# Performance work log

Hardware: AMD Instinct MI355X
Metric: run time of the kernel (lower is better)

Reference implementation:

```python
import jax, jax.numpy as jnp
import numpy as np

NODES_PER_GRAPH = 116
HEADS = 2
D_HEAD = 116  # out_channels per head
HID = 256
B = 512
N = B * NODES_PER_GRAPH
DEG = 8
E = N * DEG
D_OUT = HEADS * D_HEAD  # 232


def setup_inputs() -> dict:
    key = jax.random.key(0)
    ks = jax.random.split(key, 6)
    h_flat = jax.random.normal(ks[0], (N, HID), dtype=jnp.float32)
    # every node receives DEG edges from random nodes within its own 116-node graph
    dst = jnp.repeat(jnp.arange(N, dtype=jnp.int64), DEG)
    offs = jax.random.randint(ks[1], (E,), 0, NODES_PER_GRAPH, dtype=jnp.int64)
    src = (dst // NODES_PER_GRAPH) * NODES_PER_GRAPH + offs
    edge_index = jnp.stack([src, dst], axis=0)
    batch_index = jnp.repeat(jnp.arange(B, dtype=jnp.int64), NODES_PER_GRAPH)
    s = 1.0 / np.sqrt(HID)
    Wq = jax.random.normal(ks[2], (HID, D_OUT), dtype=jnp.float32) * s
    Wk = jax.random.normal(ks[3], (HID, D_OUT), dtype=jnp.float32) * s
    Wv = jax.random.normal(ks[4], (HID, D_OUT), dtype=jnp.float32) * s
    Ws = jax.random.normal(ks[5], (HID, D_OUT), dtype=jnp.float32) * s
    return {"h_flat": h_flat, "edge_index": edge_index, "batch_index": batch_index,
            "Wq": Wq, "Wk": Wk, "Wv": Wv, "Ws": Ws}


def _graph_transformer_layer(h, edge_index, Wq, Wk, Wv, Ws):
    # PyG TransformerConv-style multi-head edge attention, concat heads + root skip.
    n = h.shape[0]
    q = (h @ Wq).reshape(n, HEADS, D_HEAD)
    k = (h @ Wk).reshape(n, HEADS, D_HEAD)
    v = (h @ Wv).reshape(n, HEADS, D_HEAD)
    src, dst = edge_index[0], edge_index[1]
    # per-edge scores [E, H]
    scores = jnp.einsum('ehd,ehd->eh', q[dst], k[src]) / np.sqrt(D_HEAD)
    # segment softmax over incoming edges of each dst node
    m = jax.ops.segment_max(scores, dst, num_segments=n)
    m = jnp.where(jnp.isfinite(m), m, 0.0)
    ex = jnp.exp(scores - m[dst])
    denom = jax.ops.segment_sum(ex, dst, num_segments=n)
    alpha_e = ex / (denom[dst] + 1e-16)
    msg = alpha_e[:, :, None] * v[src]                      # [E, H, Dh]
    attn = jax.ops.segment_sum(msg, dst, num_segments=n)    # [N, H, Dh]
    return attn.reshape(n, D_OUT) + h @ Ws


def reference(h_flat, edge_index, batch_index, Wq, Wk, Wv, Ws):
    n = h_flat.shape[0]
    b = n // NODES_PER_GRAPH
    h_proj = _graph_transformer_layer(h_flat, edge_index, Wq, Wk, Wv, Ws)  # [N, 232]
    e = h_proj.mean(axis=-1)                                 # [N]
    # scatter_softmax over per-graph node segments
    em = jax.ops.segment_max(e, batch_index, num_segments=b)
    ee = jnp.exp(e - em[batch_index])
    es = jax.ops.segment_sum(ee, batch_index, num_segments=b)
    alpha = ee / es[batch_index]                             # [N]
    h_weighted = alpha[:, None] * h_proj                     # [N, 232]
    alpha_map = alpha.reshape(b, NODES_PER_GRAPH)            # [B, 116]
    return alpha_map, h_weighted
```

## Files before the change

### kernel.cpp

```cpp
#include <hip/hip_runtime.h>

#define NODES  116
#define HEADS  2
#define DH     116
#define HID    256
#define NGRAPH 512
#define NN     (NGRAPH*NODES)
#define DEG    8
#define DOUT   (HEADS*DH)
#define RSTR   136

typedef short  s8v  __attribute__((ext_vector_type(8)));
typedef float  f4v  __attribute__((ext_vector_type(4)));

static __device__ __forceinline__ float bf2f(unsigned short u) {
    union { unsigned int i; float f; } c; c.i = ((unsigned int)u) << 16; return c.f;
}
static __device__ __forceinline__ unsigned short f2bf(float f) {
    union { float f; unsigned int u; } c; c.f = f;
    unsigned int u = c.u;
    unsigned int r = (u + 0x7FFFu + ((u >> 16) & 1u)) >> 16;
    return (unsigned short)r;
}

#define GLD_LDS16(gptr, lptr) \
    __builtin_amdgcn_global_load_lds((const __attribute__((address_space(1))) void*)(gptr), \
                                     (__attribute__((address_space(3))) void*)(lptr), 16, 0, 0)

__global__ __launch_bounds__(256) void prep_w(const float* __restrict__ Wq,
                                              const float* __restrict__ Wk,
                                              const float* __restrict__ Wv,
                                              const float* __restrict__ Ws,
                                              unsigned short* __restrict__ wt)
{
    unsigned int f = blockIdx.x * 256 + threadIdx.x;
    unsigned int n    = f & 127;
    unsigned int quad = (f >> 7) & 3;
    unsigned int kb   = (f >> 9) & 7;
    unsigned int ch   = (f >> 12) & 3;
    unsigned int hd   = f >> 14;
    unsigned short o[8] = {0,0,0,0,0,0,0,0};
    if (n < NODES) {
        unsigned int col = hd * DH + n;
        unsigned int k   = kb * 32 + quad * 8;
        const float* W = (ch == 0) ? Wq : (ch == 1) ? Wk : (ch == 2) ? Wv : Ws;
        #pragma unroll
        for (int i = 0; i < 8; i++)
            o[i] = f2bf(W[(size_t)(k + i) * DOUT + col]);
    }
    *(uint4*)(wt + (size_t)f * 8) = *(const uint4*)o;
}

__global__ __launch_bounds__(1024) void fused_all(
    const float* __restrict__ h,
    const unsigned short* __restrict__ wt,
    const int* __restrict__ eidx,
    unsigned short* __restrict__ hp,
    float* __restrict__ out_alpha,
    float* __restrict__ out_hw)
{
    __shared__ __align__(16) unsigned short stA[2*4096];
    __shared__ __align__(16) unsigned short stB[2*16384];
    __shared__ __align__(16) unsigned short ql[128*RSTR];
    __shared__ __align__(16) unsigned short kl[128*RSTR];
    __shared__ int   srcl[NODES*DEG];
    __shared__ float scf[NODES*DEG];
    __shared__ float ps[2][NODES];
    __shared__ float red[2];

    const int g   = blockIdx.x;
    const int tid = threadIdx.x;
    const int w    = tid >> 6;
    const int lane = tid & 63;
    const int l15  = lane & 15;
    const int quad = lane >> 4;
    const int wm   = w >> 2;
    const int wn   = w & 3;

    if (tid < NODES * DEG)
        srcl[tid] = eidx[(size_t)g * NODES * DEG + tid] - g * NODES;

    const int am = tid >> 3;
    const int q8 = tid & 7;
    long grow = (long)g * NODES + am;
    if (grow >= NN) grow = NN - 1;
    const float* hrow = h + (size_t)grow * HID + q8 * 4;
    const int aoff = ((q8 >> 1) * 128 + am) * 8 + (q8 & 1) * 4;

    for (int hd = 0; hd < 2; hd++) {
        const size_t wbase = (size_t)hd * 4 * 8 * 4096;

        f4v accq[2][2], acck[2][2], accv[2][2], accs[2][2];
        #pragma unroll
        for (int i = 0; i < 2; i++)
            #pragma unroll
            for (int j = 0; j < 2; j++)
                #pragma unroll
                for (int r = 0; r < 4; r++) {
                    accq[i][j][r] = 0.f; acck[i][j][r] = 0.f;
                    accv[i][j][r] = 0.f; accs[i][j][r] = 0.f;
                }

        {
            float4 av = *(const float4*)(hrow);
            #pragma unroll
            for (int j = 0; j < 2; j++) {
                int c = w * 2 + j;
                int ch = c >> 3, sub = c & 7;
                const unsigned short* src = wt + wbase + ((size_t)(ch * 8 + 0)) * 4096 + sub * 512;
                GLD_LDS16((const char*)src + lane * 16, (char*)stB + c * 1024);
            }
            unsigned short o[4] = { f2bf(av.x), f2bf(av.y), f2bf(av.z), f2bf(av.w) };
            *(uint2*)(stA + aoff) = *(const uint2*)o;
        }
        __syncthreads();

        int cur = 0;
        for (int kb = 0; kb < 8; kb++) {
            float4 av;
            if (kb < 7) {
                av = *(const float4*)(hrow + (kb + 1) * 32);
                #pragma unroll
                for (int j = 0; j < 2; j++) {
                    int c = w * 2 + j;
                    int ch = c >> 3, sub = c & 7;
                    const unsigned short* src = wt + wbase + ((size_t)(ch * 8 + kb + 1)) * 4096 + sub * 512;
                    GLD_LDS16((const char*)src + lane * 16,
                              (char*)stB + (cur ^ 1) * 32768 + c * 1024);
                }
            }
            const unsigned short* sa = stA + cur * 4096;
            const unsigned short* sb = stB + cur * 16384;
            s8v a0 = *(const s8v*)(sa + (quad * 128 + wm * 32 + l15) * 8);
            s8v a1 = *(const s8v*)(sa + (quad * 128 + wm * 32 + 16 + l15) * 8);
            #pragma unroll
            for (int ch = 0; ch < 4; ch++) {
                s8v b0 = *(const s8v*)(sb + ch * 4096 + (quad * 128 + wn * 32 + l15) * 8);
                s8v b1 = *(const s8v*)(sb + ch * 4096 + (quad * 128 + wn * 32 + 16 + l15) * 8);
                f4v (*acc)[2] = (ch == 0) ? accq : (ch == 1) ? acck : (ch == 2) ? accv : accs;
                acc[0][0] = __builtin_amdgcn_mfma_f32_16x16x32_bf16(a0, b0, acc[0][0], 0, 0, 0);
                acc[0][1] = __builtin_amdgcn_mfma_f32_16x16x32_bf16(a0, b1, acc[0][1], 0, 0, 0);
                acc[1][0] = __builtin_amdgcn_mfma_f32_16x16x32_bf16(a1, b0, acc[1][0], 0, 0, 0);
                acc[1][1] = __builtin_amdgcn_mfma_f32_16x16x32_bf16(a1, b1, acc[1][1], 0, 0, 0);
            }
            if (kb < 7) {
                unsigned short o[4] = { f2bf(av.x), f2bf(av.y), f2bf(av.z), f2bf(av.w) };
                *(uint2*)(stA + (cur ^ 1) * 4096 + aoff) = *(const uint2*)o;
            }
            __syncthreads();
            cur ^= 1;
        }

        #pragma unroll
        for (int i = 0; i < 2; i++) {
            #pragma unroll
            for (int j = 0; j < 2; j++) {
                int col = wn * 32 + j * 16 + l15;
                #pragma unroll
                for (int r = 0; r < 4; r++) {
                    int row = wm * 32 + i * 16 + quad * 4 + r;
                    ql[row * RSTR + col] = (col < NODES) ? f2bf(accq[i][j][r]) : 0;
                    kl[row * RSTR + col] = (col < NODES) ? f2bf(acck[i][j][r]) : 0;
                }
            }
        }
        __syncthreads();

        f4v sacc[2][2];
        #pragma unroll
        for (int i = 0; i < 2; i++)
            #pragma unroll
            for (int j = 0; j < 2; j++)
                #pragma unroll
                for (int r = 0; r < 4; r++) sacc[i][j][r] = 0.f;
        #pragma unroll
        for (int ks = 0; ks < 4; ks++) {
            s8v a0 = *(const s8v*)(ql + (wm * 32 + l15) * RSTR + ks * 32 + quad * 8);
            s8v a1 = *(const s8v*)(ql + (wm * 32 + 16 + l15) * RSTR + ks * 32 + quad * 8);
            s8v b0 = *(const s8v*)(kl + (wn * 32 + l15) * RSTR + ks * 32 + quad * 8);
            s8v b1 = *(const s8v*)(kl + (wn * 32 + 16 + l15) * RSTR + ks * 32 + quad * 8);
            sacc[0][0] = __builtin_amdgcn_mfma_f32_16x16x32_bf16(a0, b0, sacc[0][0], 0, 0, 0);
            sacc[0][1] = __builtin_amdgcn_mfma_f32_16x16x32_bf16(a0, b1, sacc[0][1], 0, 0, 0);
            sacc[1][0] = __builtin_amdgcn_mfma_f32_16x16x32_bf16(a1, b0, sacc[1][0], 0, 0, 0);
            sacc[1][1] = __builtin_amdgcn_mfma_f32_16x16x32_bf16(a1, b1, sacc[1][1], 0, 0, 0);
        }
        #pragma unroll
        for (int i = 0; i < 2; i++) {
            #pragma unroll
            for (int r = 0; r < 4; r++) {
                int row = wm * 32 + i * 16 + quad * 4 + r;
                if (row < NODES) {
                    #pragma unroll
                    for (int j = 0; j < 2; j++) {
                        int col = wn * 32 + j * 16 + l15;
                        #pragma unroll
                        for (int e = 0; e < DEG; e++)
                            if (srcl[row * DEG + e] == col)
                                scf[row * DEG + e] = sacc[i][j][r];
                    }
                }
            }
        }
        __syncthreads();

        for (int f = tid; f < 128 * RSTR / 8; f += 1024)
            *(uint4*)(kl + (size_t)f * 8) = make_uint4(0u, 0u, 0u, 0u);
        #pragma unroll
        for (int i = 0; i < 2; i++) {
            #pragma unroll
            for (int j = 0; j < 2; j++) {
                int col = wn * 32 + j * 16 + l15;
                #pragma unroll
                for (int r = 0; r < 4; r++) {
                    int row = wm * 32 + i * 16 + quad * 4 + r;
                    ql[col * RSTR + row] = (row < NODES) ? f2bf(accv[i][j][r]) : 0;
                }
            }
        }
        __syncthreads();

        if (tid < NODES * DEG) {
            float s = scf[tid] * 0.09284766908852594f;
            float m = s;
            m = fmaxf(m, __shfl_xor(m, 1));
            m = fmaxf(m, __shfl_xor(m, 2));
            m = fmaxf(m, __shfl_xor(m, 4));
            float e = __expf(s - m);
            float sum = e;
            sum += __shfl_xor(sum, 1);
            sum += __shfl_xor(sum, 2);
            sum += __shfl_xor(sum, 4);
            scf[tid] = e / sum;
        }
        __syncthreads();

        if (tid < NODES) {
            #pragma unroll
            for (int j = 0; j < DEG; j++) {
                int sj = srcl[tid * DEG + j];
                bool first = true;
                for (int jj = 0; jj < j; jj++) first = first && (srcl[tid * DEG + jj] != sj);
                if (first) {
                    float a = scf[tid * DEG + j];
                    for (int jj = j + 1; jj < DEG; jj++)
                        if (srcl[tid * DEG + jj] == sj) a += scf[tid * DEG + jj];
                    kl[tid * RSTR + sj] = f2bf(a);
                }
            }
        }
        __syncthreads();

        #pragma unroll
        for (int ks = 0; ks < 4; ks++) {
            s8v a0 = *(const s8v*)(kl + (wm * 32 + l15) * RSTR + ks * 32 + quad * 8);
            s8v a1 = *(const s8v*)(kl + (wm * 32 + 16 + l15) * RSTR + ks * 32 + quad * 8);
            s8v b0 = *(const s8v*)(ql + (wn * 32 + l15) * RSTR + ks * 32 + quad * 8);
            s8v b1 = *(const s8v*)(ql + (wn * 32 + 16 + l15) * RSTR + ks * 32 + quad * 8);
            accs[0][0] = __builtin_amdgcn_mfma_f32_16x16x32_bf16(a0, b0, accs[0][0], 0, 0, 0);
            accs[0][1] = __builtin_amdgcn_mfma_f32_16x16x32_bf16(a0, b1, accs[0][1], 0, 0, 0);
            accs[1][0] = __builtin_amdgcn_mfma_f32_16x16x32_bf16(a1, b0, accs[1][0], 0, 0, 0);
            accs[1][1] = __builtin_amdgcn_mfma_f32_16x16x32_bf16(a1, b1, accs[1][1], 0, 0, 0);
        }
        __syncthreads();

        #pragma unroll
        for (int i = 0; i < 2; i++) {
            #pragma unroll
            for (int j = 0; j < 2; j++) {
                int col = wn * 32 + j * 16 + l15;
                #pragma unroll
                for (int r = 0; r < 4; r++) {
                    int row = wm * 32 + i * 16 + quad * 4 + r;
                    ql[row * RSTR + col] = f2bf(accs[i][j][r]);
                }
            }
        }
        __syncthreads();

        if (tid < NODES * DEG) {
            const int i   = tid >> 3;
            const int seg = tid & 7;
            float rs = 0.0f;
            #pragma unroll
            for (int t = 0; t < 2; t++) {
                int gi = seg + t * 8;
                if (gi < 15) {
                    const s8v v8 = *(const s8v*)(ql + i * RSTR + gi * 8);
                    #pragma unroll
                    for (int e = 0; e < 8; e++) rs += bf2f((unsigned short)v8[e]);
                }
            }
            rs += __shfl_xor(rs, 1);
            rs += __shfl_xor(rs, 2);
            rs += __shfl_xor(rs, 4);
            if (seg == 0) ps[hd][i] = rs;
        }
        if (hd == 0) {
            for (int f = tid; f < NODES * 29; f += 1024) {
                int r  = f / 29;
                int gi = f - r * 29;
                *(uint2*)(hp + ((size_t)g * NODES + r) * 116 + gi * 4) =
                    *(const uint2*)(ql + r * RSTR + gi * 4);
            }
        }
        __syncthreads();
    }

    if (tid < NODES) scf[tid] = (ps[0][tid] + ps[1][tid]) * (1.0f / DOUT);
    __syncthreads();
    if (tid < 64) {
        float a = scf[tid];
        float b = (tid + 64 < NODES) ? scf[tid + 64] : -1e30f;
        float mm = fmaxf(a, b);
        #pragma unroll
        for (int off = 32; off > 0; off >>= 1) mm = fmaxf(mm, __shfl_down(mm, off));
        if (tid == 0) red[0] = mm;
    }
    __syncthreads();
    if (tid < NODES) scf[tid] = __expf(scf[tid] - red[0]);
    __syncthreads();
    if (tid < 64) {
        float a = scf[tid] + ((tid + 64 < NODES) ? scf[tid + 64] : 0.0f);
        #pragma unroll
        for (int off = 32; off > 0; off >>= 1) a += __shfl_down(a, off);
        if (tid == 0) red[1] = a;
    }
    __syncthreads();
    if (tid < NODES) {
        float al = scf[tid] / red[1];
        scf[tid] = al;
        out_alpha[(size_t)g * NODES + tid] = al;
    }
    __syncthreads();
    for (int f = tid; f < NODES * 58; f += 1024) {
        int r  = f / 58;
        int gi = f - r * 58;
        float al = scf[r];
        float4 o;
        if (gi < 29) {
            uint2 hv = *(const uint2*)(hp + ((size_t)g * NODES + r) * 116 + gi * 4);
            o = make_float4(al * bf2f((unsigned short)(hv.x & 0xFFFF)),
                            al * bf2f((unsigned short)(hv.x >> 16)),
                            al * bf2f((unsigned short)(hv.y & 0xFFFF)),
                            al * bf2f((unsigned short)(hv.y >> 16)));
        } else {
            const unsigned short* hv = ql + r * RSTR + (gi - 29) * 4;
            o = make_float4(al * bf2f(hv[0]), al * bf2f(hv[1]),
                            al * bf2f(hv[2]), al * bf2f(hv[3]));
        }
        *(float4*)(out_hw + ((size_t)g * NODES + r) * DOUT + gi * 4) = o;
    }
}

extern "C" void kernel_launch(void* const* d_in, const int* in_sizes, int n_in,
                              void* d_out, int out_size, void* d_ws, size_t ws_size,
                              hipStream_t stream)
{
    const float* h    = (const float*)d_in[0];
    const int*   eidx = (const int*)d_in[1];
    const float* Wq   = (const float*)d_in[3];
    const float* Wk   = (const float*)d_in[4];
    const float* Wv   = (const float*)d_in[5];
    const float* Ws   = (const float*)d_in[6];

    unsigned short* wt = (unsigned short*)d_ws;
    unsigned short* hp = wt + (size_t)262144;

    float* out_alpha = (float*)d_out;
    float* out_hw    = out_alpha + NN;

    prep_w<<<128, 256, 0, stream>>>(Wq, Wk, Wv, Ws, wt);
    fused_all<<<NGRAPH, 1024, 0, stream>>>(h, wt, eidx, hp, out_alpha, out_hw);
}
```

Baseline: 246.9 us.

## Preload full bf16 A tile once, single-buffer weights, alias kl with weight stage

Loads and converts the whole 116x256 h tile into LDS once up front, so it is reused by both heads instead of being reloaded from global memory per head. The weight staging buffer becomes single-buffered and shares storage with the kl buffer, and the head loop is unrolled. This removes the duplicate h loads and the conditional prefetch logic. In exchange the weight load for each k-step is no longer overlapped with the MFMA work, and each step adds an extra barrier.

```diff
diff --git a/kernel.cpp b/kernel.cpp
--- a/kernel.cpp
+++ b/kernel.cpp
@@ -59,14 +59,16 @@
     float* __restrict__ out_alpha,
     float* __restrict__ out_hw)
 {
-    __shared__ __align__(16) unsigned short stA[2*4096];
-    __shared__ __align__(16) unsigned short stB[2*16384];
+    __shared__ __align__(16) unsigned short stA[8*4096];
+    __shared__ __align__(16) unsigned short xreg[17408];
     __shared__ __align__(16) unsigned short ql[128*RSTR];
-    __shared__ __align__(16) unsigned short kl[128*RSTR];
     __shared__ int   srcl[NODES*DEG];
     __shared__ float scf[NODES*DEG];
     __shared__ float ps[2][NODES];
     __shared__ float red[2];
+
+    unsigned short* const stB = xreg;
+    unsigned short* const kl  = xreg;
 
     const int g   = blockIdx.x;
     const int tid = threadIdx.x;
@@ -80,13 +82,25 @@
     if (tid < NODES * DEG)
         srcl[tid] = eidx[(size_t)g * NODES * DEG + tid] - g * NODES;
 
-    const int am = tid >> 3;
-    const int q8 = tid & 7;
-    long grow = (long)g * NODES + am;
-    if (grow >= NN) grow = NN - 1;
-    const float* hrow = h + (size_t)grow * HID + q8 * 4;
-    const int aoff = ((q8 >> 1) * 128 + am) * 8 + (q8 & 1) * 4;
-
+    {
+        const int am = tid >> 3;
+        const int q8 = tid & 7;
+        long grow = (long)g * NODES + am;
+        if (grow >= NN) grow = NN - 1;
+        const float* hrow = h + (size_t)grow * HID + q8 * 4;
+        const int aoff = ((q8 >> 1) * 128 + am) * 8 + (q8 & 1) * 4;
+        float4 a8[8];
+        #pragma unroll
+        for (int kb = 0; kb < 8; kb++) a8[kb] = *(const float4*)(hrow + kb * 32);
+        #pragma unroll
+        for (int kb = 0; kb < 8; kb++) {
+            unsigned short o[4] = { f2bf(a8[kb].x), f2bf(a8[kb].y),
+                                    f2bf(a8[kb].z), f2bf(a8[kb].w) };
+            *(uint2*)(stA + kb * 4096 + aoff) = *(const uint2*)o;
+        }
+    }
+
+    #pragma unroll
     for (int hd = 0; hd < 2; hd++) {
         const size_t wbase = (size_t)hd * 4 * 8 * 4096;
 
@@ -101,54 +115,31 @@
                     accv[i][j][r] = 0.f; accs[i][j][r] = 0.f;
                 }
 
-        {
-            float4 av = *(const float4*)(hrow);
+        for (int kb = 0; kb < 8; kb++) {
             #pragma unroll
             for (int j = 0; j < 2; j++) {
                 int c = w * 2 + j;
                 int ch = c >> 3, sub = c & 7;
-                const unsigned short* src = wt + wbase + ((size_t)(ch * 8 + 0)) * 4096 + sub * 512;
+                const unsigned short* src = wt + wbase + ((size_t)(ch * 8 + kb)) * 4096 + sub * 512;
                 GLD_LDS16((const char*)src + lane * 16, (char*)stB + c * 1024);
             }
-            unsigned short o[4] = { f2bf(av.x), f2bf(av.y), f2bf(av.z), f2bf(av.w) };
-            *(uint2*)(stA + aoff) = *(const uint2*)o;
-        }
-        __syncthreads();
-
-        int cur = 0;
-        for (int kb = 0; kb < 8; kb++) {
-            float4 av;
-            if (kb < 7) {
-                av = *(const float4*)(hrow + (kb + 1) * 32);
-                #pragma unroll
-                for (int j = 0; j < 2; j++) {
-                    int c = w * 2 + j;
-                    int ch = c >> 3, sub = c & 7;
-                    const unsigned short* src = wt + wbase + ((size_t)(ch * 8 + kb + 1)) * 4096 + sub * 512;
-                    GLD_LDS16((const char*)src + lane * 16,
-                              (char*)stB + (cur ^ 1) * 32768 + c * 1024);
-                }
-            }
-            const unsigned short* sa = stA + cur * 4096;
-            const unsigned short* sb = stB + cur * 16384;
+            __syncthreads();
+            const unsigned short* sa = stA + kb * 4096;
             s8v a0 = *(const s8v*)(sa + (quad * 128 + wm * 32 + l15) * 8);
             s8v a1 = *(const s8v*)(sa + (quad * 128 + wm * 32 + 16 + l15) * 8);
-            #pragma unroll
-            for (int ch = 0; ch < 4; ch++) {
-                s8v b0 = *(const s8v*)(sb + ch * 4096 + (quad * 128 + wn * 32 + l15) * 8);
-                s8v b1 = *(const s8v*)(sb + ch * 4096 + (quad * 128 + wn * 32 + 16 + l15) * 8);
-                f4v (*acc)[2] = (ch == 0) ? accq : (ch == 1) ? acck : (ch == 2) ? accv : accs;
-                acc[0][0] = __builtin_amdgcn_mfma_f32_16x16x32_bf16(a0, b0, acc[0][0], 0, 0, 0);
-                acc[0][1] = __builtin_amdgcn_mfma_f32_16x16x32_bf16(a0, b1, acc[0][1], 0, 0, 0);
-                acc[1][0] = __builtin_amdgcn_mfma_f32_16x16x32_bf16(a1, b0, acc[1][0], 0, 0, 0);
-                acc[1][1] = __builtin_amdgcn_mfma_f32_16x16x32_bf16(a1, b1, acc[1][1], 0, 0, 0);
-            }
-            if (kb < 7) {
-                unsigned short o[4] = { f2bf(av.x), f2bf(av.y), f2bf(av.z), f2bf(av.w) };
-                *(uint2*)(stA + (cur ^ 1) * 4096 + aoff) = *(const uint2*)o;
-            }
+            #define CHUNK_MFMA(ACC, CH) { \
+                s8v b0 = *(const s8v*)(stB + (CH) * 4096 + (quad * 128 + wn * 32 + l15) * 8); \
+                s8v b1 = *(const s8v*)(stB + (CH) * 4096 + (quad * 128 + wn * 32 + 16 + l15) * 8); \
+                ACC[0][0] = __builtin_amdgcn_mfma_f32_16x16x32_bf16(a0, b0, ACC[0][0], 0, 0, 0); \
+                ACC[0][1] = __builtin_amdgcn_mfma_f32_16x16x32_bf16(a0, b1, ACC[0][1], 0, 0, 0); \
+                ACC[1][0] = __builtin_amdgcn_mfma_f32_16x16x32_bf16(a1, b0, ACC[1][0], 0, 0, 0); \
+                ACC[1][1] = __builtin_amdgcn_mfma_f32_16x16x32_bf16(a1, b1, ACC[1][1], 0, 0, 0); }
+            CHUNK_MFMA(accq, 0)
+            CHUNK_MFMA(acck, 1)
+            CHUNK_MFMA(accv, 2)
+            CHUNK_MFMA(accs, 3)
+            #undef CHUNK_MFMA
             __syncthreads();
-            cur ^= 1;
         }
 
         #pragma unroll
```

Measured after the change: 221.9 us. 10.1% less time.
